# Kernel optimization log

Measured on AMD Instinct MI355X. Metric: run time of the kernel, lower is better.

Reference implementation:

```python
import jax, jax.numpy as jnp
import numpy as np

N, D_IN, E, H, F, T = 50000, 128, 800000, 8, 32, 8
NEG_SLOPE = 0.2


def setup_inputs() -> dict:
    key = jax.random.key(0)
    ks = jax.random.split(key, 12)
    feat = jax.random.normal(ks[0], (N, D_IN), dtype=jnp.float32)
    edge_embeddings = jax.random.normal(ks[1], (E, H), dtype=jnp.float32)
    src = jax.random.randint(ks[2], (E,), 0, N, dtype=jnp.int32)
    dst = jnp.sort(jax.random.randint(ks[3], (E,), 0, N, dtype=jnp.int32))
    etype = jax.random.randint(ks[4], (E,), 0, T, dtype=jnp.int32)
    s = 0.05
    W_src = jax.random.normal(ks[5], (H * F, D_IN), dtype=jnp.float32) * s
    attn_l = jax.random.normal(ks[6], (1, H, F), dtype=jnp.float32) * s
    attn_r = jax.random.normal(ks[7], (1, H, F), dtype=jnp.float32) * s
    attn_e = jax.random.normal(ks[8], (1, H, F), dtype=jnp.float32) * s
    W_e = jax.random.normal(ks[9], (H * F, H), dtype=jnp.float32) * s
    type_emb = jax.random.normal(ks[10], (T, F), dtype=jnp.float32) * s
    k2 = jax.random.split(ks[11], 3)
    W_et = jax.random.normal(k2[0], (H * F, F), dtype=jnp.float32) * s
    attn_et = jax.random.normal(k2[1], (1, H, F), dtype=jnp.float32) * s
    bias = jnp.zeros((H * F,), dtype=jnp.float32)
    return dict(feat=feat, edge_embeddings=edge_embeddings, src=src, dst=dst,
                etype=etype, W_src=W_src, attn_l=attn_l, attn_r=attn_r,
                attn_e=attn_e, W_e=W_e, type_emb=type_emb, W_et=W_et,
                attn_et=attn_et, bias=bias)


def _leaky_relu(x):
    return jnp.where(x >= 0, x, NEG_SLOPE * x)


def reference(feat, edge_embeddings, src, dst, etype, W_src, attn_l, attn_r,
              attn_e, W_e, type_emb, W_et, attn_et, bias):
    n = feat.shape[0]
    # node transform (shared src/dst weights)
    fs = (feat @ W_src.T).reshape(n, H, F)           # [N,H,F]
    el = (fs * attn_l).sum(-1)                        # [N,H]
    er = (fs * attn_r).sum(-1)                        # [N,H]
    e = el[src] + er[dst]                             # [E,H] (u_add_v)
    # edge embedding attention term
    ee = (edge_embeddings @ W_e.T).reshape(-1, H, F)  # [E,H,F]
    e_score = (ee * attn_e).sum(-1)                   # [E,H]
    # edge type embedding attention term
    te = type_emb[etype]                              # [E,F]
    te = (te @ W_et.T).reshape(-1, H, F)              # [E,H,F]
    t_score = (te * attn_et).sum(-1)                  # [E,H]
    attn = e + e_score + t_score                      # attn_agg = sum
    # edge-type frequency normalization
    counts = jnp.bincount(etype, length=T).astype(jnp.float32)
    w = counts.sum() / (T * counts)                   # [T]
    attn = attn * w[etype][:, None]
    attn = _leaky_relu(attn)                          # v2=False -> after agg
    # edge softmax over incoming edges of each dst node
    m = jax.ops.segment_max(attn, dst, num_segments=n)  # [N,H]
    a = jnp.exp(attn - m[dst])
    z = jax.ops.segment_sum(a, dst, num_segments=n)     # [N,H]
    a = a / z[dst]                                      # [E,H]
    # weighted scatter aggregation
    msg = fs[src] * a[:, :, None]                       # [E,H,F]
    out = jax.ops.segment_sum(msg, dst, num_segments=n) # [N,H,F]
    return out + bias.reshape(1, H, F)
```

## Files before the change

### kernel.cpp

```cpp
#include <hip/hip_runtime.h>
#include <math.h>

#define N_NODES 50000
#define D_IN    128
#define E_EDGES 800000
#define H_HEADS 8
#define F_FEAT  32
#define T_TYPES 8
#define HF      256
#define NEG_SLOPE 0.2f
#define HIST_BLOCKS 256

using short8 = __attribute__((__ext_vector_type__(8))) short;
using f32x4  = __attribute__((__ext_vector_type__(4))) float;

__device__ inline float bf2f(unsigned short u) {
    union { unsigned int i; float f; } v; v.i = ((unsigned int)u) << 16; return v.f;
}
__device__ inline unsigned short f2bf(float f) {
    unsigned int x = __float_as_uint(f);
    unsigned int r = (x + 0x7fffu + ((x >> 16) & 1u)) >> 16;
    return (unsigned short)r;
}
__device__ inline unsigned int pk2bf(float a, float b) {
    return (unsigned int)f2bf(a) | ((unsigned int)f2bf(b) << 16);
}

__global__ __launch_bounds__(256) void hist_part(const int* __restrict__ etype,
                                                 int* __restrict__ partials) {
    __shared__ int sw[4][8];
    int c[8] = {0,0,0,0,0,0,0,0};
    const int stride = gridDim.x * blockDim.x;
    for (int e = blockIdx.x * blockDim.x + threadIdx.x; e < E_EDGES; e += stride) {
        int ty = etype[e];
#pragma unroll
        for (int t = 0; t < 8; ++t) c[t] += (ty == t) ? 1 : 0;
    }
#pragma unroll
    for (int t = 0; t < 8; ++t) {
        c[t] += __shfl_xor(c[t], 1);  c[t] += __shfl_xor(c[t], 2);
        c[t] += __shfl_xor(c[t], 4);  c[t] += __shfl_xor(c[t], 8);
        c[t] += __shfl_xor(c[t], 16); c[t] += __shfl_xor(c[t], 32);
    }
    const int wid = threadIdx.x >> 6, l = threadIdx.x & 63;
    if (l == 0) {
#pragma unroll
        for (int t = 0; t < 8; ++t) sw[wid][t] = c[t];
    }
    __syncthreads();
    if (threadIdx.x < 8) {
        int t = threadIdx.x;
        partials[blockIdx.x * 8 + t] = sw[0][t] + sw[1][t] + sw[2][t] + sw[3][t];
    }
}

__global__ __launch_bounds__(256) void tables_kernel(const float* __restrict__ attn_e,
                              const float* __restrict__ W_e,
                              const float* __restrict__ attn_et,
                              const float* __restrict__ W_et,
                              const float* __restrict__ type_emb,
                              const int* __restrict__ partials,
                              float* __restrict__ M, float* __restrict__ ttab,
                              float* __restrict__ w) {
    __shared__ float q[8][32];
    int t = threadIdx.x;
    {
        int h = t >> 5, f2 = t & 31;
        float s = 0.f;
#pragma unroll 8
        for (int f = 0; f < F_FEAT; ++f)
            s += attn_et[h * 32 + f] * W_et[(h * 32 + f) * 32 + f2];
        q[h][f2] = s;
    }
    __syncthreads();
    if (t < 64) {
        int h = t >> 3, j = t & 7;
        float m = 0.f;
#pragma unroll 8
        for (int f = 0; f < F_FEAT; ++f)
            m += attn_e[h * 32 + f] * W_e[(h * 32 + f) * 8 + j];
        M[h * 8 + j] = m;
        float tt = 0.f;
#pragma unroll 8
        for (int f2 = 0; f2 < F_FEAT; ++f2)
            tt += type_emb[j * 32 + f2] * q[h][f2];
        ttab[j * 8 + h] = tt;
    }
    if (t < 64) {
        int j = t & 7, chunk = t >> 3;
        int c = 0;
#pragma unroll 8
        for (int b = 0; b < HIST_BLOCKS / 8; ++b)
            c += partials[(chunk * (HIST_BLOCKS / 8) + b) * 8 + j];
        c += __shfl_xor(c, 8); c += __shfl_xor(c, 16); c += __shfl_xor(c, 32);
        if (t < 8) {
            if (c < 1) c = 1;
            w[t] = (float)E_EDGES / (8.0f * (float)c);
        }
    }
}

__global__ __launch_bounds__(256) void node_gemm(const float* __restrict__ feat,
                                                 const float* __restrict__ W,
                                                 const float* __restrict__ attn_l,
                                                 const float* __restrict__ attn_r,
                                                 unsigned short* __restrict__ fsb,
                                                 float* __restrict__ el,
                                                 float* __restrict__ er) {
    __shared__ unsigned short Wl[HF * D_IN];
    const int t = threadIdx.x;
    for (int i = 0; i < 16; ++i) {
        int slot = i * 256 + t;
        int n = slot >> 4, k16 = slot & 15;
        const float* wp = W + (size_t)n * D_IN + k16 * 8;
        float4 w0 = *(const float4*)wp;
        float4 w1 = *(const float4*)(wp + 4);
        union { unsigned int u[4]; short8 s; } ua;
        ua.u[0] = pk2bf(w0.x, w0.y); ua.u[1] = pk2bf(w0.z, w0.w);
        ua.u[2] = pk2bf(w1.x, w1.y); ua.u[3] = pk2bf(w1.z, w1.w);
        int idx = n * D_IN + ((k16 * 8) ^ ((n & 7) << 3));
        *(short8*)&Wl[idx] = ua.s;
    }
    __syncthreads();

    const int wid = t >> 6, l = t & 63;
    const int r16 = l & 15, kq = l >> 4;
    const int node0 = blockIdx.x * 64 + wid * 16;
    int arow = node0 + r16;
    if (arow >= N_NODES) arow = N_NODES - 1;
    const float* fp = feat + (size_t)arow * D_IN + kq * 8;

    f32x4 acc[16];
#pragma unroll
    for (int i = 0; i < 16; ++i) acc[i] = (f32x4){0.f, 0.f, 0.f, 0.f};

#pragma unroll
    for (int kc = 0; kc < 4; ++kc) {
        float4 a0 = *(const float4*)(fp + kc * 32);
        float4 a1 = *(const float4*)(fp + kc * 32 + 4);
        union { unsigned int u[4]; short8 s; } ua;
        ua.u[0] = pk2bf(a0.x, a0.y); ua.u[1] = pk2bf(a0.z, a0.w);
        ua.u[2] = pk2bf(a1.x, a1.y); ua.u[3] = pk2bf(a1.z, a1.w);
        short8 af = ua.s;
#pragma unroll
        for (int nsub = 0; nsub < 16; ++nsub) {
            int n = nsub * 16 + r16;
            int idx = n * D_IN + ((kc * 32 + kq * 8) ^ ((n & 7) << 3));
            short8 bf = *(short8*)&Wl[idx];
            acc[nsub] = __builtin_amdgcn_mfma_f32_16x16x32_bf16(af, bf, acc[nsub], 0, 0, 0);
        }
    }

    const int nodeb = node0 + kq * 4;
#pragma unroll
    for (int h = 0; h < 8; ++h) {
        float al0 = attn_l[h * 32 + r16],      al1 = attn_l[h * 32 + 16 + r16];
        float ar0 = attn_r[h * 32 + r16],      ar1 = attn_r[h * 32 + 16 + r16];
        float ev[4], rv[4];
#pragma unroll
        for (int g = 0; g < 4; ++g) {
            ev[g] = acc[2 * h][g] * al0 + acc[2 * h + 1][g] * al1;
            rv[g] = acc[2 * h][g] * ar0 + acc[2 * h + 1][g] * ar1;
        }
#pragma unroll
        for (int g = 0; g < 4; ++g) {
            ev[g] += __shfl_xor(ev[g], 1); ev[g] += __shfl_xor(ev[g], 2);
            ev[g] += __shfl_xor(ev[g], 4); ev[g] += __shfl_xor(ev[g], 8);
            rv[g] += __shfl_xor(rv[g], 1); rv[g] += __shfl_xor(rv[g], 2);
            rv[g] += __shfl_xor(rv[g], 4); rv[g] += __shfl_xor(rv[g], 8);
        }
        if (r16 == 0) {
#pragma unroll
            for (int g = 0; g < 4; ++g) {
                int nd = nodeb + g;
                if (nd < N_NODES) {
                    el[nd * 8 + h] = ev[g];
                    er[nd * 8 + h] = rv[g];
                }
            }
        }
    }
#pragma unroll
    for (int nsub = 0; nsub < 16; ++nsub) {
        int col = nsub * 16 + r16;
#pragma unroll
        for (int g = 0; g < 4; ++g) {
            int nd = nodeb + g;
            if (nd < N_NODES) fsb[(size_t)nd * HF + col] = f2bf(acc[nsub][g]);
        }
    }
}

__global__ __launch_bounds__(256) void build_offsets(const int* __restrict__ dst,
                                                     int* __restrict__ off) {
    int n = blockIdx.x * blockDim.x + threadIdx.x;
    if (n > N_NODES) return;
    int lo = 0, hi = E_EDGES;
    while (lo < hi) {
        int mid = (lo + hi) >> 1;
        if (dst[mid] < n) lo = mid + 1; else hi = mid;
    }
    off[n] = lo;
}

__global__ __launch_bounds__(256) void edge_kernel(const float* __restrict__ ee,
        const int* __restrict__ src, const int* __restrict__ dst,
        const int* __restrict__ etype, const float* __restrict__ el,
        const float* __restrict__ er, const float* __restrict__ M,
        const float* __restrict__ ttab, const float* __restrict__ w,
        unsigned short* __restrict__ pexp) {
    __shared__ float sM[64], sT[64], sw[8];
    int t = threadIdx.x;
    if (t < 64) { sM[t] = M[t]; sT[t] = ttab[t]; }
    if (t < 8) sw[t] = w[t];
    __syncthreads();
    int e = blockIdx.x * 256 + t;
    if (e >= E_EDGES) return;
    int s = src[e], d = dst[e], ty = etype[e];
    float4 e0 = *(const float4*)&ee[(size_t)e * 8];
    float4 e1 = *(const float4*)&ee[(size_t)e * 8 + 4];
    float4 l0 = *(const float4*)&el[s * 8];
    float4 l1 = *(const float4*)&el[s * 8 + 4];
    float4 r0 = *(const float4*)&er[d * 8];
    float4 r1 = *(const float4*)&er[d * 8 + 4];
    float wt = sw[ty];
    float lv[8] = {l0.x,l0.y,l0.z,l0.w,l1.x,l1.y,l1.z,l1.w};
    float rv[8] = {r0.x,r0.y,r0.z,r0.w,r1.x,r1.y,r1.z,r1.w};
    unsigned int o[4];
#pragma unroll
    for (int hp = 0; hp < 4; ++hp) {
        float p2[2];
#pragma unroll
        for (int i = 0; i < 2; ++i) {
            int h = hp * 2 + i;
            float sc = lv[h] + rv[h] + sT[ty * 8 + h];
            sc += e0.x*sM[h*8+0] + e0.y*sM[h*8+1] + e0.z*sM[h*8+2] + e0.w*sM[h*8+3]
                + e1.x*sM[h*8+4] + e1.y*sM[h*8+5] + e1.z*sM[h*8+6] + e1.w*sM[h*8+7];
            sc *= wt;
            sc = (sc >= 0.f) ? sc : NEG_SLOPE * sc;
            p2[i] = __expf(sc);
        }
        o[hp] = (unsigned int)f2bf(p2[0]) | ((unsigned int)f2bf(p2[1]) << 16);
    }
    *(uint4*)&pexp[(size_t)e * 8] = make_uint4(o[0], o[1], o[2], o[3]);
}

__global__ __launch_bounds__(256) void agg_kernel(const unsigned short* __restrict__ pexp,
        const unsigned short* __restrict__ fsb, const int* __restrict__ src,
        const int* __restrict__ off, const float* __restrict__ bias,
        float* __restrict__ out) {
    const int wid = threadIdx.x >> 6;
    const int l = threadIdx.x & 63;
    const int n = blockIdx.x * 4 + wid;
    if (n >= N_NODES) return;
    const int beg = off[n], end = off[n + 1];
    const int c0 = 4 * l;
    const int h = l >> 3;
    const float4 b4 = *(const float4*)&bias[c0];
    float* op = &out[(size_t)n * HF + c0];
    if (beg == end) { *(float4*)op = b4; return; }
    float a0 = 0.f, a1 = 0.f, a2 = 0.f, a3 = 0.f, z = 0.f;
    for (int base = beg; base < end; base += 64) {
        const int remn = end - base;
        const int rem = remn < 64 ? remn : 64;
        int idx = base + l; if (idx >= end) idx = end - 1;
        const int sl = src[idx];
        int j = 0;
        for (; j + 4 <= rem; j += 4) {
            const int s0 = __shfl(sl, j);
            const int s1 = __shfl(sl, j + 1);
            const int s2 = __shfl(sl, j + 2);
            const int s3 = __shfl(sl, j + 3);
            const float p0 = bf2f(pexp[(size_t)(base + j) * 8 + h]);
            const float p1 = bf2f(pexp[(size_t)(base + j + 1) * 8 + h]);
            const float p2 = bf2f(pexp[(size_t)(base + j + 2) * 8 + h]);
            const float p3 = bf2f(pexp[(size_t)(base + j + 3) * 8 + h]);
            const ushort4 f0 = *(const ushort4*)&fsb[(size_t)s0 * HF + c0];
            const ushort4 f1 = *(const ushort4*)&fsb[(size_t)s1 * HF + c0];
            const ushort4 f2 = *(const ushort4*)&fsb[(size_t)s2 * HF + c0];
            const ushort4 f3 = *(const ushort4*)&fsb[(size_t)s3 * HF + c0];
            a0 += p0 * bf2f(f0.x); a1 += p0 * bf2f(f0.y);
            a2 += p0 * bf2f(f0.z); a3 += p0 * bf2f(f0.w); z += p0;
            a0 += p1 * bf2f(f1.x); a1 += p1 * bf2f(f1.y);
            a2 += p1 * bf2f(f1.z); a3 += p1 * bf2f(f1.w); z += p1;
            a0 += p2 * bf2f(f2.x); a1 += p2 * bf2f(f2.y);
            a2 += p2 * bf2f(f2.z); a3 += p2 * bf2f(f2.w); z += p2;
            a0 += p3 * bf2f(f3.x); a1 += p3 * bf2f(f3.y);
            a2 += p3 * bf2f(f3.z); a3 += p3 * bf2f(f3.w); z += p3;
        }
        for (; j < rem; ++j) {
            const int s0 = __shfl(sl, j);
            const float p0 = bf2f(pexp[(size_t)(base + j) * 8 + h]);
            const ushort4 f0 = *(const ushort4*)&fsb[(size_t)s0 * HF + c0];
            a0 += p0 * bf2f(f0.x); a1 += p0 * bf2f(f0.y);
            a2 += p0 * bf2f(f0.z); a3 += p0 * bf2f(f0.w); z += p0;
        }
    }
    const float rz = 1.f / z;
    *(float4*)op = make_float4(a0 * rz + b4.x, a1 * rz + b4.y,
                               a2 * rz + b4.z, a3 * rz + b4.w);
}

extern "C" void kernel_launch(void* const* d_in, const int* in_sizes, int n_in,
                              void* d_out, int out_size, void* d_ws, size_t ws_size,
                              hipStream_t stream) {
    const float* feat     = (const float*)d_in[0];
    const float* ee       = (const float*)d_in[1];
    const int*   src      = (const int*)d_in[2];
    const int*   dst      = (const int*)d_in[3];
    const int*   etype    = (const int*)d_in[4];
    const float* W_src    = (const float*)d_in[5];
    const float* attn_l   = (const float*)d_in[6];
    const float* attn_r   = (const float*)d_in[7];
    const float* attn_e   = (const float*)d_in[8];
    const float* W_e      = (const float*)d_in[9];
    const float* type_emb = (const float*)d_in[10];
    const float* W_et     = (const float*)d_in[11];
    const float* attn_et  = (const float*)d_in[12];
    const float* bias     = (const float*)d_in[13];
    float* out = (float*)d_out;

    char* ws = (char*)d_ws;
    size_t o = 0;
    auto alloc = [&](size_t bytes) -> void* {
        void* p = ws + o;
        o = (o + bytes + 255) & ~(size_t)255;
        return p;
    };
    unsigned short* fsb  = (unsigned short*)alloc((size_t)N_NODES * HF * 2);
    unsigned short* pexp = (unsigned short*)alloc((size_t)E_EDGES * 8 * 2);
    float* el    = (float*)alloc((size_t)N_NODES * 8 * 4);
    float* er    = (float*)alloc((size_t)N_NODES * 8 * 4);
    int*   off   = (int*)alloc((size_t)(N_NODES + 1) * 4);
    int*   partials = (int*)alloc((size_t)HIST_BLOCKS * 8 * 4);
    float* M     = (float*)alloc(64 * 4);
    float* ttab  = (float*)alloc(64 * 4);
    float* w     = (float*)alloc(T_TYPES * 4);

    hist_part<<<HIST_BLOCKS, 256, 0, stream>>>(etype, partials);
    tables_kernel<<<1, 256, 0, stream>>>(attn_e, W_e, attn_et, W_et, type_emb,
                                         partials, M, ttab, w);
    node_gemm<<<(N_NODES + 63) / 64, 256, 0, stream>>>(feat, W_src, attn_l, attn_r,
                                                       fsb, el, er);
    build_offsets<<<(N_NODES + 1 + 255) / 256, 256, 0, stream>>>(dst, off);
    edge_kernel<<<(E_EDGES + 255) / 256, 256, 0, stream>>>(
        ee, src, dst, etype, el, er, M, ttab, w, pexp);
    agg_kernel<<<(N_NODES + 3) / 4, 256, 0, stream>>>(pexp, fsb, src, off, bias, out);
}
```

Before: 128.3 us.

## Merge histogram, node GEMM and offset build into one persistent prep kernel

Fuses the etype histogram, node projection GEMM and dst offset binary search into a single launch with block-range dispatch. The GEMM part becomes persistent over 208 blocks, so the bf16 weight tile in shared memory is loaded once per block instead of once per 64-node group, and the attention vectors are hoisted into registers. This removes two kernel launches and repeated weight staging. The aggregation inner loop is also unrolled from 4 to 8 edges so more gathers are in flight, at the cost of more registers.

```diff
diff --git a/kernel.cpp b/kernel.cpp
--- a/kernel.cpp
+++ b/kernel.cpp
@@ -10,6 +10,12 @@
 #define HF      256
 #define NEG_SLOPE 0.2f
 #define HIST_BLOCKS 256
+#define GEMM_BLOCKS 208
+#define OFF_BLOCKS  196
+#define K1_HIST_BASE GEMM_BLOCKS
+#define K1_OFF_BASE  (GEMM_BLOCKS + HIST_BLOCKS)
+#define K1_GRID      (GEMM_BLOCKS + HIST_BLOCKS + OFF_BLOCKS)
+#define NGROUPS      ((N_NODES + 63) / 64)
 
 using short8 = __attribute__((__ext_vector_type__(8))) short;
 using f32x4  = __attribute__((__ext_vector_type__(4))) float;
@@ -26,31 +32,143 @@
     return (unsigned int)f2bf(a) | ((unsigned int)f2bf(b) << 16);
 }
 
-__global__ __launch_bounds__(256) void hist_part(const int* __restrict__ etype,
-                                                 int* __restrict__ partials) {
+__global__ __launch_bounds__(256) void prep_kernel(const float* __restrict__ feat,
+                                                   const float* __restrict__ W,
+                                                   const float* __restrict__ attn_l,
+                                                   const float* __restrict__ attn_r,
+                                                   const int*   __restrict__ etype,
+                                                   const int*   __restrict__ dst,
+                                                   unsigned short* __restrict__ fsb,
+                                                   float* __restrict__ el,
+                                                   float* __restrict__ er,
+                                                   int* __restrict__ partials,
+                                                   int* __restrict__ off) {
+    __shared__ unsigned short Wl[HF * D_IN];
     __shared__ int sw[4][8];
-    int c[8] = {0,0,0,0,0,0,0,0};
-    const int stride = gridDim.x * blockDim.x;
-    for (int e = blockIdx.x * blockDim.x + threadIdx.x; e < E_EDGES; e += stride) {
-        int ty = etype[e];
-#pragma unroll
-        for (int t = 0; t < 8; ++t) c[t] += (ty == t) ? 1 : 0;
-    }
-#pragma unroll
-    for (int t = 0; t < 8; ++t) {
-        c[t] += __shfl_xor(c[t], 1);  c[t] += __shfl_xor(c[t], 2);
-        c[t] += __shfl_xor(c[t], 4);  c[t] += __shfl_xor(c[t], 8);
-        c[t] += __shfl_xor(c[t], 16); c[t] += __shfl_xor(c[t], 32);
-    }
-    const int wid = threadIdx.x >> 6, l = threadIdx.x & 63;
-    if (l == 0) {
-#pragma unroll
-        for (int t = 0; t < 8; ++t) sw[wid][t] = c[t];
+    const int t = threadIdx.x;
+
+    if (blockIdx.x >= K1_OFF_BASE) {
+        int n = (blockIdx.x - K1_OFF_BASE) * 256 + t;
+        if (n > N_NODES) return;
+        int lo = 0, hi = E_EDGES;
+        while (lo < hi) {
+            int mid = (lo + hi) >> 1;
+            if (dst[mid] < n) lo = mid + 1; else hi = mid;
+        }
+        off[n] = lo;
+        return;
+    }
+    if (blockIdx.x >= K1_HIST_BASE) {
+        const int hb = blockIdx.x - K1_HIST_BASE;
+        int c[8] = {0,0,0,0,0,0,0,0};
+        const int stride = HIST_BLOCKS * 256;
+        for (int e = hb * 256 + t; e < E_EDGES; e += stride) {
+            int ty = etype[e];
+#pragma unroll
+            for (int k = 0; k < 8; ++k) c[k] += (ty == k) ? 1 : 0;
+        }
+#pragma unroll
+        for (int k = 0; k < 8; ++k) {
+            c[k] += __shfl_xor(c[k], 1);  c[k] += __shfl_xor(c[k], 2);
+            c[k] += __shfl_xor(c[k], 4);  c[k] += __shfl_xor(c[k], 8);
+            c[k] += __shfl_xor(c[k], 16); c[k] += __shfl_xor(c[k], 32);
+        }
+        const int wv = t >> 6, l = t & 63;
+        if (l == 0) {
+#pragma unroll
+            for (int k = 0; k < 8; ++k) sw[wv][k] = c[k];
+        }
+        __syncthreads();
+        if (t < 8) partials[hb * 8 + t] = sw[0][t] + sw[1][t] + sw[2][t] + sw[3][t];
+        return;
+    }
+
+    for (int i = 0; i < 16; ++i) {
+        int slot = i * 256 + t;
+        int n = slot >> 4, k16 = slot & 15;
+        const float* wp = W + (size_t)n * D_IN + k16 * 8;
+        float4 w0 = *(const float4*)wp;
+        float4 w1 = *(const float4*)(wp + 4);
+        union { unsigned int u[4]; short8 s; } ua;
+        ua.u[0] = pk2bf(w0.x, w0.y); ua.u[1] = pk2bf(w0.z, w0.w);
+        ua.u[2] = pk2bf(w1.x, w1.y); ua.u[3] = pk2bf(w1.z, w1.w);
+        int idx = n * D_IN + ((k16 * 8) ^ ((n & 7) << 3));
+        *(short8*)&Wl[idx] = ua.s;
     }
     __syncthreads();
-    if (threadIdx.x < 8) {
-        int t = threadIdx.x;
-        partials[blockIdx.x * 8 + t] = sw[0][t] + sw[1][t] + sw[2][t] + sw[3][t];
+
+    const int wid = t >> 6, l = t & 63;
+    const int r16 = l & 15, kq = l >> 4;
+    float alv0[8], alv1[8], arv0[8], arv1[8];
+#pragma unroll
+    for (int h = 0; h < 8; ++h) {
+        alv0[h] = attn_l[h * 32 + r16];  alv1[h] = attn_l[h * 32 + 16 + r16];
+        arv0[h] = attn_r[h * 32 + r16];  arv1[h] = attn_r[h * 32 + 16 + r16];
+    }
+
+    for (int grp = blockIdx.x; grp < NGROUPS; grp += GEMM_BLOCKS) {
+        const int node0 = grp * 64 + wid * 16;
+        int arow = node0 + r16;
+        if (arow >= N_NODES) arow = N_NODES - 1;
+        const float* fp = feat + (size_t)arow * D_IN + kq * 8;
+
+        f32x4 acc[16];
+#pragma unroll
+        for (int i = 0; i < 16; ++i) acc[i] = (f32x4){0.f, 0.f, 0.f, 0.f};
+
+#pragma unroll
+        for (int kc = 0; kc < 4; ++kc) {
+            float4 a0 = *(const float4*)(fp + kc * 32);
+            float4 a1 = *(const float4*)(fp + kc * 32 + 4);
+            union { unsigned int u[4]; short8 s; } ua;
+            ua.u[0] = pk2bf(a0.x, a0.y); ua.u[1] = pk2bf(a0.z, a0.w);
+            ua.u[2] = pk2bf(a1.x, a1.y); ua.u[3] = pk2bf(a1.z, a1.w);
+            short8 af = ua.s;
+#pragma unroll
+            for (int nsub = 0; nsub < 16; ++nsub) {
+                int n = nsub * 16 + r16;
+                int idx = n * D_IN + ((kc * 32 + kq * 8) ^ ((n & 7) << 3));
+                short8 bf = *(short8*)&Wl[idx];
+                acc[nsub] = __builtin_amdgcn_mfma_f32_16x16x32_bf16(af, bf, acc[nsub], 0, 0, 0);
+            }
+        }
+
+        const int nodeb = node0 + kq * 4;
+#pragma unroll
+        for (int h = 0; h < 8; ++h) {
+            float ev[4], rv[4];
+#pragma unroll
+            for (int g = 0; g < 4; ++g) {
+                ev[g] = acc[2 * h][g] * alv0[h] + acc[2 * h + 1][g] * alv1[h];
+                rv[g] = acc[2 * h][g] * arv0[h] + acc[2 * h + 1][g] * arv1[h];
+            }
+#pragma unroll
+            for (int g = 0; g < 4; ++g) {
+                ev[g] += __shfl_xor(ev[g], 1); ev[g] += __shfl_xor(ev[g], 2);
+                ev[g] += __shfl_xor(ev[g], 4); ev[g] += __shfl_xor(ev[g], 8);
+                rv[g] += __shfl_xor(rv[g], 1); rv[g] += __shfl_xor(rv[g], 2);
+                rv[g] += __shfl_xor(rv[g], 4); rv[g] += __shfl_xor(rv[g], 8);
+            }
+            if (r16 == 0) {
+#pragma unroll
+                for (int g = 0; g < 4; ++g) {
+                    int nd = nodeb + g;
+                    if (nd < N_NODES) {
+                        el[nd * 8 + h] = ev[g];
+                        er[nd * 8 + h] = rv[g];
+                    }
+                }
+            }
+        }
+#pragma unroll
+        for (int nsub = 0; nsub < 16; ++nsub) {
+            int col = nsub * 16 + r16;
+#pragma unroll
+            for (int g = 0; g < 4; ++g) {
+                int nd = nodeb + g;
+                if (nd < N_NODES) fsb[(size_t)nd * HF + col] = f2bf(acc[nsub][g]);
+            }
+        }
     }
 }
 
@@ -98,109 +216,6 @@
             w[t] = (float)E_EDGES / (8.0f * (float)c);
         }
     }
-}
-
-__global__ __launch_bounds__(256) void node_gemm(const float* __restrict__ feat,
-                                                 const float* __restrict__ W,
-                                                 const float* __restrict__ attn_l,
-                                                 const float* __restrict__ attn_r,
-                                                 unsigned short* __restrict__ fsb,
-                                                 float* __restrict__ el,
-                                                 float* __restrict__ er) {
-    __shared__ unsigned short Wl[HF * D_IN];
-    const int t = threadIdx.x;
-    for (int i = 0; i < 16; ++i) {
-        int slot = i * 256 + t;
-        int n = slot >> 4, k16 = slot & 15;
-        const float* wp = W + (size_t)n * D_IN + k16 * 8;
-        float4 w0 = *(const float4*)wp;
-        float4 w1 = *(const float4*)(wp + 4);
-        union { unsigned int u[4]; short8 s; } ua;
-        ua.u[0] = pk2bf(w0.x, w0.y); ua.u[1] = pk2bf(w0.z, w0.w);
-        ua.u[2] = pk2bf(w1.x, w1.y); ua.u[3] = pk2bf(w1.z, w1.w);
-        int idx = n * D_IN + ((k16 * 8) ^ ((n & 7) << 3));
-        *(short8*)&Wl[idx] = ua.s;
-    }
-    __syncthreads();
-
-    const int wid = t >> 6, l = t & 63;
-    const int r16 = l & 15, kq = l >> 4;
-    const int node0 = blockIdx.x * 64 + wid * 16;
-    int arow = node0 + r16;
-    if (arow >= N_NODES) arow = N_NODES - 1;
-    const float* fp = feat + (size_t)arow * D_IN + kq * 8;
-
-    f32x4 acc[16];
-#pragma unroll
-    for (int i = 0; i < 16; ++i) acc[i] = (f32x4){0.f, 0.f, 0.f, 0.f};
-
-#pragma unroll
-    for (int kc = 0; kc < 4; ++kc) {
-        float4 a0 = *(const float4*)(fp + kc * 32);
-        float4 a1 = *(const float4*)(fp + kc * 32 + 4);
-        union { unsigned int u[4]; short8 s; } ua;
-        ua.u[0] = pk2bf(a0.x, a0.y); ua.u[1] = pk2bf(a0.z, a0.w);
-        ua.u[2] = pk2bf(a1.x, a1.y); ua.u[3] = pk2bf(a1.z, a1.w);
-        short8 af = ua.s;
-#pragma unroll
-        for (int nsub = 0; nsub < 16; ++nsub) {
-            int n = nsub * 16 + r16;
-            int idx = n * D_IN + ((kc * 32 + kq * 8) ^ ((n & 7) << 3));
-            short8 bf = *(short8*)&Wl[idx];
-            acc[nsub] = __builtin_amdgcn_mfma_f32_16x16x32_bf16(af, bf, acc[nsub], 0, 0, 0);
-        }
-    }
-
-    const int nodeb = node0 + kq * 4;
-#pragma unroll
-    for (int h = 0; h < 8; ++h) {
-        float al0 = attn_l[h * 32 + r16],      al1 = attn_l[h * 32 + 16 + r16];
-        float ar0 = attn_r[h * 32 + r16],      ar1 = attn_r[h * 32 + 16 + r16];
-        float ev[4], rv[4];
-#pragma unroll
-        for (int g = 0; g < 4; ++g) {
-            ev[g] = acc[2 * h][g] * al0 + acc[2 * h + 1][g] * al1;
-            rv[g] = acc[2 * h][g] * ar0 + acc[2 * h + 1][g] * ar1;
-        }
-#pragma unroll
-        for (int g = 0; g < 4; ++g) {
-            ev[g] += __shfl_xor(ev[g], 1); ev[g] += __shfl_xor(ev[g], 2);
-            ev[g] += __shfl_xor(ev[g], 4); ev[g] += __shfl_xor(ev[g], 8);
-            rv[g] += __shfl_xor(rv[g], 1); rv[g] += __shfl_xor(rv[g], 2);
-            rv[g] += __shfl_xor(rv[g], 4); rv[g] += __shfl_xor(rv[g], 8);
-        }
-        if (r16 == 0) {
-#pragma unroll
-            for (int g = 0; g < 4; ++g) {
-                int nd = nodeb + g;
-                if (nd < N_NODES) {
-                    el[nd * 8 + h] = ev[g];
-                    er[nd * 8 + h] = rv[g];
-                }
-            }
-        }
-    }
-#pragma unroll
-    for (int nsub = 0; nsub < 16; ++nsub) {
-        int col = nsub * 16 + r16;
-#pragma unroll
-        for (int g = 0; g < 4; ++g) {
-            int nd = nodeb + g;
-            if (nd < N_NODES) fsb[(size_t)nd * HF + col] = f2bf(acc[nsub][g]);
-        }
-    }
-}
-
-__global__ __launch_bounds__(256) void build_offsets(const int* __restrict__ dst,
-                                                     int* __restrict__ off) {
-    int n = blockIdx.x * blockDim.x + threadIdx.x;
-    if (n > N_NODES) return;
-    int lo = 0, hi = E_EDGES;
-    while (lo < hi) {
-        int mid = (lo + hi) >> 1;
-        if (dst[mid] < n) lo = mid + 1; else hi = mid;
-    }
-    off[n] = lo;
 }
 
 __global__ __launch_bounds__(256) void edge_kernel(const float* __restrict__ ee,
@@ -266,27 +281,22 @@
         int idx = base + l; if (idx >= end) idx = end - 1;
         const int sl = src[idx];
         int j = 0;
-        for (; j + 4 <= rem; j += 4) {
-            const int s0 = __shfl(sl, j);
-            const int s1 = __shfl(sl, j + 1);
-            const int s2 = __shfl(sl, j + 2);
-            const int s3 = __shfl(sl, j + 3);
-            const float p0 = bf2f(pexp[(size_t)(base + j) * 8 + h]);
-            const float p1 = bf2f(pexp[(size_t)(base + j + 1) * 8 + h]);
-            const float p2 = bf2f(pexp[(size_t)(base + j + 2) * 8 + h]);
-            const float p3 = bf2f(pexp[(size_t)(base + j + 3) * 8 + h]);
-            const ushort4 f0 = *(const ushort4*)&fsb[(size_t)s0 * HF + c0];
-            const ushort4 f1 = *(const ushort4*)&fsb[(size_t)s1 * HF + c0];
-            const ushort4 f2 = *(const ushort4*)&fsb[(size_t)s2 * HF + c0];
-            const ushort4 f3 = *(const ushort4*)&fsb[(size_t)s3 * HF + c0];
-            a0 += p0 * bf2f(f0.x); a1 += p0 * bf2f(f0.y);
-            a2 += p0 * bf2f(f0.z); a3 += p0 * bf2f(f0.w); z += p0;
-            a0 += p1 * bf2f(f1.x); a1 += p1 * bf2f(f1.y);
-            a2 += p1 * bf2f(f1.z); a3 += p1 * bf2f(f1.w); z += p1;
-            a0 += p2 * bf2f(f2.x); a1 += p2 * bf2f(f2.y);
-            a2 += p2 * bf2f(f2.z); a3 += p2 * bf2f(f2.w); z += p2;
-            a0 += p3 * bf2f(f3.x); a1 += p3 * bf2f(f3.y);
-            a2 += p3 * bf2f(f3.z); a3 += p3 * bf2f(f3.w); z += p3;
+        for (; j + 8 <= rem; j += 8) {
+            int   ss[8]; float pp[8]; ushort4 ff[8];
+#pragma unroll
+            for (int u = 0; u < 8; ++u) ss[u] = __shfl(sl, j + u);
+#pragma unroll
+            for (int u = 0; u < 8; ++u)
+                pp[u] = bf2f(pexp[(size_t)(base + j + u) * 8 + h]);
+#pragma unroll
+            for (int u = 0; u < 8; ++u)
+                ff[u] = *(const ushort4*)&fsb[(size_t)ss[u] * HF + c0];
+#pragma unroll
+            for (int u = 0; u < 8; ++u) {
+                a0 += pp[u] * bf2f(ff[u].x); a1 += pp[u] * bf2f(ff[u].y);
+                a2 += pp[u] * bf2f(ff[u].z); a3 += pp[u] * bf2f(ff[u].w);
+                z += pp[u];
+            }
         }
         for (; j < rem; ++j) {
             const int s0 = __shfl(sl, j);
@@ -337,12 +347,11 @@
     float* ttab  = (float*)alloc(64 * 4);
     float* w     = (float*)alloc(T_TYPES * 4);
 
-    hist_part<<<HIST_BLOCKS, 256, 0, stream>>>(etype, partials);
+    prep_kernel<<<K1_GRID, 256, 0, stream>>>(feat, W_src, attn_l, attn_r,
+                                             etype, dst, fsb, el, er,
+                                             partials, off);
     tables_kernel<<<1, 256, 0, stream>>>(attn_e, W_e, attn_et, W_et, type_emb,
                                          partials, M, ttab, w);
-    node_gemm<<<(N_NODES + 63) / 64, 256, 0, stream>>>(feat, W_src, attn_l, attn_r,
-                                                       fsb, el, er);
-    build_offsets<<<(N_NODES + 1 + 255) / 256, 256, 0, stream>>>(dst, off);
     edge_kernel<<<(E_EDGES + 255) / 256, 256, 0, stream>>>(
         ee, src, dst, etype, el, er, M, ttab, w, pexp);
     agg_kernel<<<(N_NODES + 3) / 4, 256, 0, stream>>>(pexp, fsb, src, off, bias, out);
```

Result: no change. 128.6 us (+0.2%).
